# Kernel tuning notes

Measured on AMD Instinct MI355X. Metric: run time of the kernel, lower is better.

The kernel has to match this reference:

```python
import jax, jax.numpy as jnp
import numpy as np

WINDOW_SIZE = 3
SIGMA = 1.5
C1 = 0.01 ** 2
C2 = 0.03 ** 2


def gaussian_window(channel, window_size=WINDOW_SIZE, sigma=SIGMA):
    x = jnp.arange(window_size, dtype=jnp.float32) - window_size // 2
    g1 = jnp.exp(-(x ** 2) / (2.0 * sigma ** 2))
    g1 = g1 / g1.sum()
    g2 = jnp.outer(g1, g1)  # [k, k]
    # depthwise kernel OIHW: [C, 1, k, k]
    return jnp.broadcast_to(g2, (channel, 1, window_size, window_size))


def depthwise_conv(x, window, channel, window_size=WINDOW_SIZE):
    pad = window_size // 2
    return jax.lax.conv_general_dilated(
        x, window,
        window_strides=(1, 1),
        padding=((pad, pad), (pad, pad)),
        dimension_numbers=('NCHW', 'OIHW', 'NCHW'),
        feature_group_count=channel,
    )


def setup_inputs() -> dict:
    key = jax.random.key(0)
    k1, k2 = jax.random.split(key)
    img1 = jax.random.uniform(k1, (32, 3, 512, 512), dtype=jnp.float32)
    img2 = jax.random.uniform(k2, (32, 3, 512, 512), dtype=jnp.float32)
    return {"img1": img1, "img2": img2}


def reference(img1, img2):
    channel = img1.shape[1]
    window = gaussian_window(channel)

    mu1 = depthwise_conv(img1, window, channel)
    mu2 = depthwise_conv(img2, window, channel)
    mu1_sq = mu1 * mu1
    mu2_sq = mu2 * mu2
    mu1_mu2 = mu1 * mu2

    sigma1_sq = depthwise_conv(img1 * img1, window, channel) - mu1_sq
    sigma2_sq = depthwise_conv(img2 * img2, window, channel) - mu2_sq
    sigma12 = depthwise_conv(img1 * img2, window, channel) - mu1_mu2

    ssim_map = ((2.0 * mu1_mu2 + C1) * (2.0 * sigma12 + C2)) / (
        (mu1_sq + mu2_sq + C1) * (sigma1_sq + sigma2_sq + C2))

    # size_sum defaults to True inside ssim() -> scalar sum
    return 1.0 - ssim_map.sum()
```

## Files before the change

kernel.cpp:

```cpp
#include <hip/hip_runtime.h>

#define IMG_H 512
#define IMG_W 512
#define RH 32

__global__ void ssim_init_kernel(double* __restrict__ accum) {
    if (threadIdx.x == 0 && blockIdx.x == 0) *accum = 0.0;
}

__global__ __launch_bounds__(256) void ssim_main_kernel(
    const float* __restrict__ img1, const float* __restrict__ img2,
    double* __restrict__ accum)
{
    constexpr float W_E = 0.30780133f;
    constexpr float W_C = 0.38439734f;
    constexpr float C1 = 1e-4f;
    constexpr float C2 = 9e-4f;

    const int t = threadIdx.x;
    const int y0 = blockIdx.x * RH;
    const size_t base = (size_t)blockIdx.y * (IMG_H * IMG_W);
    const float* __restrict__ A = img1 + base;
    const float* __restrict__ B = img2 + base;

    __shared__ __align__(16) float lsA[2][520];
    __shared__ __align__(16) float lsB[2][520];
    if (t < 2) {
        lsA[0][t * 513] = 0.0f; lsA[1][t * 513] = 0.0f;
        lsB[0][t * 513] = 0.0f; lsB[1][t * 513] = 0.0f;
    }

    const int x = 2 * t;

    float h1[2][3], h2[2][3], h11[2][3], h22[2][3], h12[2][3];
#pragma unroll
    for (int c = 0; c < 2; ++c)
#pragma unroll
        for (int r = 0; r < 3; ++r) {
            h1[c][r] = 0.f; h2[c][r] = 0.f;
            h11[c][r] = 0.f; h22[c][r] = 0.f; h12[c][r] = 0.f;
        }

    float2 pa = make_float2(0.f, 0.f), pb = make_float2(0.f, 0.f);
    {
        const int yi = y0 - 1;
        if (yi >= 0) {
            pa = *(const float2*)(A + (size_t)yi * IMG_W + x);
            pb = *(const float2*)(B + (size_t)yi * IMG_W + x);
        }
    }

    float tsum = 0.0f;

    for (int i = 0; i < RH + 2; ++i) {
        const int buf = i & 1;
        lsA[buf][1 + x] = pa.x; lsA[buf][2 + x] = pa.y;
        lsB[buf][1 + x] = pb.x; lsB[buf][2 + x] = pb.y;

        const int yn = y0 + i;
        float2 na = make_float2(0.f, 0.f), nb = make_float2(0.f, 0.f);
        if (i + 1 < RH + 2 && yn < IMG_H) {
            na = *(const float2*)(A + (size_t)yn * IMG_W + x);
            nb = *(const float2*)(B + (size_t)yn * IMG_W + x);
        }

        __syncthreads();

        const float2 a01 = *(const float2*)&lsA[buf][x];
        const float2 a23 = *(const float2*)&lsA[buf][x + 2];
        const float2 b01 = *(const float2*)&lsB[buf][x];
        const float2 b23 = *(const float2*)&lsB[buf][x + 2];
        const float av[4] = {a01.x, a01.y, a23.x, a23.y};
        const float bv[4] = {b01.x, b01.y, b23.x, b23.y};

#pragma unroll
        for (int c = 0; c < 2; ++c) {
            h1[c][0] = h1[c][1];  h1[c][1] = h1[c][2];
            h2[c][0] = h2[c][1];  h2[c][1] = h2[c][2];
            h11[c][0] = h11[c][1]; h11[c][1] = h11[c][2];
            h22[c][0] = h22[c][1]; h22[c][1] = h22[c][2];
            h12[c][0] = h12[c][1]; h12[c][1] = h12[c][2];
            const float am = av[c], a0 = av[c + 1], ap = av[c + 2];
            const float bm = bv[c], b0 = bv[c + 1], bp = bv[c + 2];
            h1[c][2]  = W_E * (am + ap) + W_C * a0;
            h2[c][2]  = W_E * (bm + bp) + W_C * b0;
            h11[c][2] = W_E * (am * am + ap * ap) + W_C * (a0 * a0);
            h22[c][2] = W_E * (bm * bm + bp * bp) + W_C * (b0 * b0);
            h12[c][2] = W_E * (am * bm + ap * bp) + W_C * (a0 * b0);
        }

        if (i >= 2) {
#pragma unroll
            for (int c = 0; c < 2; ++c) {
                const float mu1 = W_E * (h1[c][0] + h1[c][2]) + W_C * h1[c][1];
                const float mu2 = W_E * (h2[c][0] + h2[c][2]) + W_C * h2[c][1];
                const float e11 = W_E * (h11[c][0] + h11[c][2]) + W_C * h11[c][1];
                const float e22 = W_E * (h22[c][0] + h22[c][2]) + W_C * h22[c][1];
                const float e12 = W_E * (h12[c][0] + h12[c][2]) + W_C * h12[c][1];
                const float mu1s = mu1 * mu1, mu2s = mu2 * mu2, m12 = mu1 * mu2;
                const float s11 = e11 - mu1s, s22 = e22 - mu2s, s12 = e12 - m12;
                const float num = (2.0f * m12 + C1) * (2.0f * s12 + C2);
                const float den = (mu1s + mu2s + C1) * (s11 + s22 + C2);
                tsum += num / den;
            }
        }

        pa = na; pb = nb;
    }

#pragma unroll
    for (int off = 32; off >= 1; off >>= 1)
        tsum += __shfl_xor(tsum, off, 64);

    __shared__ float wpart[4];
    if ((t & 63) == 0) wpart[t >> 6] = tsum;
    __syncthreads();
    if (t == 0) {
        const double bs = (double)wpart[0] + (double)wpart[1] +
                          (double)wpart[2] + (double)wpart[3];
        atomicAdd(accum, bs);
    }
}

__global__ void ssim_fin_kernel(const double* __restrict__ accum,
                                float* __restrict__ out) {
    if (threadIdx.x == 0 && blockIdx.x == 0) out[0] = 1.0f - (float)(*accum);
}

extern "C" void kernel_launch(void* const* d_in, const int* in_sizes, int n_in,
                              void* d_out, int out_size, void* d_ws, size_t ws_size,
                              hipStream_t stream) {
    const float* img1 = (const float*)d_in[0];
    const float* img2 = (const float*)d_in[1];
    float* out = (float*)d_out;
    double* accum = (double*)d_ws;

    const int planes = in_sizes[0] / (IMG_H * IMG_W);

    ssim_init_kernel<<<1, 1, 0, stream>>>(accum);
    dim3 grid(IMG_H / RH, planes);
    ssim_main_kernel<<<grid, 256, 0, stream>>>(img1, img2, accum);
    ssim_fin_kernel<<<1, 1, 0, stream>>>(accum, out);
}
```

Measured before the change: 229.2 us.

## Replace LDS halo exchange with direct global loads and per-block partial sums

Removes the shared-memory row staging and the per-row __syncthreads, so each thread loads its own left and right halo pixels straight from global memory (cache-served). The row loop is unrolled by six with register rotation, which removes the h-array shifts. The double atomic accumulator and its init kernel are replaced by per-block partial writes and a parallel reduction in the final kernel, saving one launch. The trade-off is extra scalar global loads per row, plus a launch_bounds occupancy hint.

```diff
diff --git a/kernel.cpp b/kernel.cpp
--- a/kernel.cpp
+++ b/kernel.cpp
@@ -4,127 +4,138 @@
 #define IMG_W 512
 #define RH 32
 
-__global__ void ssim_init_kernel(double* __restrict__ accum) {
-    if (threadIdx.x == 0 && blockIdx.x == 0) *accum = 0.0;
-}
 
-__global__ __launch_bounds__(256) void ssim_main_kernel(
+__global__ __launch_bounds__(256, 6) void ssim_main_kernel(
     const float* __restrict__ img1, const float* __restrict__ img2,
-    double* __restrict__ accum)
+    double* __restrict__ partial)
 {
     constexpr float W_E = 0.30780133f;
     constexpr float W_C = 0.38439734f;
-    constexpr float C1 = 1e-4f;
-    constexpr float C2 = 9e-4f;
+    constexpr float C1c = 1e-4f;
+    constexpr float C2c = 9e-4f;
 
     const int t = threadIdx.x;
     const int y0 = blockIdx.x * RH;
-    const size_t base = (size_t)blockIdx.y * (IMG_H * IMG_W);
+    const size_t base = (size_t)blockIdx.y * (size_t)(IMG_H * IMG_W);
     const float* __restrict__ A = img1 + base;
     const float* __restrict__ B = img2 + base;
-
-    __shared__ __align__(16) float lsA[2][520];
-    __shared__ __align__(16) float lsB[2][520];
-    if (t < 2) {
-        lsA[0][t * 513] = 0.0f; lsA[1][t * 513] = 0.0f;
-        lsB[0][t * 513] = 0.0f; lsB[1][t * 513] = 0.0f;
-    }
-
+    const bool has_l = (t > 0);
+    const bool has_r = (t < 255);
     const int x = 2 * t;
 
     float h1[2][3], h2[2][3], h11[2][3], h22[2][3], h12[2][3];
-#pragma unroll
-    for (int c = 0; c < 2; ++c)
-#pragma unroll
-        for (int r = 0; r < 3; ++r) {
-            h1[c][r] = 0.f; h2[c][r] = 0.f;
-            h11[c][r] = 0.f; h22[c][r] = 0.f; h12[c][r] = 0.f;
-        }
-
-    float2 pa = make_float2(0.f, 0.f), pb = make_float2(0.f, 0.f);
-    {
-        const int yi = y0 - 1;
-        if (yi >= 0) {
-            pa = *(const float2*)(A + (size_t)yi * IMG_W + x);
-            pb = *(const float2*)(B + (size_t)yi * IMG_W + x);
-        }
-    }
 
     float tsum = 0.0f;
 
-    for (int i = 0; i < RH + 2; ++i) {
-        const int buf = i & 1;
-        lsA[buf][1 + x] = pa.x; lsA[buf][2 + x] = pa.y;
-        lsB[buf][1 + x] = pb.x; lsB[buf][2 + x] = pb.y;
+    float a00, a01, a02, a03, b00, b01, b02, b03;
+    float a10, a11, a12, a13, b10, b11, b12, b13;
 
-        const int yn = y0 + i;
-        float2 na = make_float2(0.f, 0.f), nb = make_float2(0.f, 0.f);
-        if (i + 1 < RH + 2 && yn < IMG_H) {
-            na = *(const float2*)(A + (size_t)yn * IMG_W + x);
-            nb = *(const float2*)(B + (size_t)yn * IMG_W + x);
-        }
+#define LOADROW(AP, BP, OFF) do {                                   \
+    const float2 _ma = *(const float2*)(A + (OFF));                 \
+    const float2 _mb = *(const float2*)(B + (OFF));                 \
+    AP##1 = _ma.x; AP##2 = _ma.y; BP##1 = _mb.x; BP##2 = _mb.y;     \
+    AP##0 = has_l ? A[(OFF) - 1] : 0.0f;                            \
+    AP##3 = has_r ? A[(OFF) + 2] : 0.0f;                            \
+    BP##0 = has_l ? B[(OFF) - 1] : 0.0f;                            \
+    BP##3 = has_r ? B[(OFF) + 2] : 0.0f;                            \
+} while (0)
 
-        __syncthreads();
+#define ZEROROW(AP, BP) do {                                        \
+    AP##0 = 0.f; AP##1 = 0.f; AP##2 = 0.f; AP##3 = 0.f;             \
+    BP##0 = 0.f; BP##1 = 0.f; BP##2 = 0.f; BP##3 = 0.f;             \
+} while (0)
 
-        const float2 a01 = *(const float2*)&lsA[buf][x];
-        const float2 a23 = *(const float2*)&lsA[buf][x + 2];
-        const float2 b01 = *(const float2*)&lsB[buf][x];
-        const float2 b23 = *(const float2*)&lsB[buf][x + 2];
-        const float av[4] = {a01.x, a01.y, a23.x, a23.y};
-        const float bv[4] = {b01.x, b01.y, b23.x, b23.y};
+#define HPASS(AP, BP, S) do {                                               \
+    const float sa0 = AP##0 * AP##0, sa1 = AP##1 * AP##1;                   \
+    const float sa2 = AP##2 * AP##2, sa3 = AP##3 * AP##3;                   \
+    const float sb0 = BP##0 * BP##0, sb1 = BP##1 * BP##1;                   \
+    const float sb2 = BP##2 * BP##2, sb3 = BP##3 * BP##3;                   \
+    const float p0 = AP##0 * BP##0, p1 = AP##1 * BP##1;                     \
+    const float p2 = AP##2 * BP##2, p3 = AP##3 * BP##3;                     \
+    h1[0][S]  = W_E * (AP##0 + AP##2) + W_C * AP##1;                        \
+    h1[1][S]  = W_E * (AP##1 + AP##3) + W_C * AP##2;                        \
+    h2[0][S]  = W_E * (BP##0 + BP##2) + W_C * BP##1;                        \
+    h2[1][S]  = W_E * (BP##1 + BP##3) + W_C * BP##2;                        \
+    h11[0][S] = W_E * (sa0 + sa2) + W_C * sa1;                              \
+    h11[1][S] = W_E * (sa1 + sa3) + W_C * sa2;                              \
+    h22[0][S] = W_E * (sb0 + sb2) + W_C * sb1;                              \
+    h22[1][S] = W_E * (sb1 + sb3) + W_C * sb2;                              \
+    h12[0][S] = W_E * (p0 + p2) + W_C * p1;                                 \
+    h12[1][S] = W_E * (p1 + p3) + W_C * p2;                                 \
+} while (0)
+
+#define VOUT(E0, E1, MID) do {                                              \
+    _Pragma("unroll")                                                       \
+    for (int c = 0; c < 2; ++c) {                                           \
+        const float mu1 = W_E * (h1[c][E0] + h1[c][E1]) + W_C * h1[c][MID]; \
+        const float mu2 = W_E * (h2[c][E0] + h2[c][E1]) + W_C * h2[c][MID]; \
+        const float e11 = W_E * (h11[c][E0] + h11[c][E1]) + W_C * h11[c][MID]; \
+        const float e22 = W_E * (h22[c][E0] + h22[c][E1]) + W_C * h22[c][MID]; \
+        const float e12 = W_E * (h12[c][E0] + h12[c][E1]) + W_C * h12[c][MID]; \
+        const float mu1s = mu1 * mu1, mu2s = mu2 * mu2, m12 = mu1 * mu2;    \
+        const float s11 = e11 - mu1s, s22 = e22 - mu2s, s12 = e12 - m12;    \
+        const float num = (2.0f * m12 + C1c) * (2.0f * s12 + C2c);          \
+        const float den = (mu1s + mu2s + C1c) * (s11 + s22 + C2c);          \
+        tsum += num / den;                                                  \
+    }                                                                       \
+} while (0)
+
+    size_t off = (size_t)y0 * IMG_W + x;
+
+    if (blockIdx.x != 0) LOADROW(a0, b0, off - IMG_W); else ZEROROW(a0, b0);
+    LOADROW(a1, b1, off);
+    HPASS(a0, b0, 0);
+    LOADROW(a0, b0, off + IMG_W);
+    HPASS(a1, b1, 1);
+    off += 2 * (size_t)IMG_W;
+
+#pragma unroll 1
+    for (int g = 0; g < 5; ++g) {
+        LOADROW(a1, b1, off); off += IMG_W; HPASS(a0, b0, 2); VOUT(2, 0, 1);
+        LOADROW(a0, b0, off); off += IMG_W; HPASS(a1, b1, 0); VOUT(0, 1, 2);
+        LOADROW(a1, b1, off); off += IMG_W; HPASS(a0, b0, 1); VOUT(1, 2, 0);
+        LOADROW(a0, b0, off); off += IMG_W; HPASS(a1, b1, 2); VOUT(2, 0, 1);
+        LOADROW(a1, b1, off); off += IMG_W; HPASS(a0, b0, 0); VOUT(0, 1, 2);
+        LOADROW(a0, b0, off); off += IMG_W; HPASS(a1, b1, 1); VOUT(1, 2, 0);
+    }
+
+    if (blockIdx.x != (IMG_H / RH - 1)) LOADROW(a1, b1, off); else ZEROROW(a1, b1);
+    HPASS(a0, b0, 2); VOUT(2, 0, 1);
+    HPASS(a1, b1, 0); VOUT(0, 1, 2);
+
+#undef LOADROW
+#undef ZEROROW
+#undef HPASS
+#undef VOUT
 
 #pragma unroll
-        for (int c = 0; c < 2; ++c) {
-            h1[c][0] = h1[c][1];  h1[c][1] = h1[c][2];
-            h2[c][0] = h2[c][1];  h2[c][1] = h2[c][2];
-            h11[c][0] = h11[c][1]; h11[c][1] = h11[c][2];
-            h22[c][0] = h22[c][1]; h22[c][1] = h22[c][2];
-            h12[c][0] = h12[c][1]; h12[c][1] = h12[c][2];
-            const float am = av[c], a0 = av[c + 1], ap = av[c + 2];
-            const float bm = bv[c], b0 = bv[c + 1], bp = bv[c + 2];
-            h1[c][2]  = W_E * (am + ap) + W_C * a0;
-            h2[c][2]  = W_E * (bm + bp) + W_C * b0;
-            h11[c][2] = W_E * (am * am + ap * ap) + W_C * (a0 * a0);
-            h22[c][2] = W_E * (bm * bm + bp * bp) + W_C * (b0 * b0);
-            h12[c][2] = W_E * (am * bm + ap * bp) + W_C * (a0 * b0);
-        }
-
-        if (i >= 2) {
-#pragma unroll
-            for (int c = 0; c < 2; ++c) {
-                const float mu1 = W_E * (h1[c][0] + h1[c][2]) + W_C * h1[c][1];
-                const float mu2 = W_E * (h2[c][0] + h2[c][2]) + W_C * h2[c][1];
-                const float e11 = W_E * (h11[c][0] + h11[c][2]) + W_C * h11[c][1];
-                const float e22 = W_E * (h22[c][0] + h22[c][2]) + W_C * h22[c][1];
-                const float e12 = W_E * (h12[c][0] + h12[c][2]) + W_C * h12[c][1];
-                const float mu1s = mu1 * mu1, mu2s = mu2 * mu2, m12 = mu1 * mu2;
-                const float s11 = e11 - mu1s, s22 = e22 - mu2s, s12 = e12 - m12;
-                const float num = (2.0f * m12 + C1) * (2.0f * s12 + C2);
-                const float den = (mu1s + mu2s + C1) * (s11 + s22 + C2);
-                tsum += num / den;
-            }
-        }
-
-        pa = na; pb = nb;
-    }
-
-#pragma unroll
-    for (int off = 32; off >= 1; off >>= 1)
-        tsum += __shfl_xor(tsum, off, 64);
+    for (int o = 32; o >= 1; o >>= 1)
+        tsum += __shfl_xor(tsum, o, 64);
 
     __shared__ float wpart[4];
     if ((t & 63) == 0) wpart[t >> 6] = tsum;
     __syncthreads();
     if (t == 0) {
-        const double bs = (double)wpart[0] + (double)wpart[1] +
-                          (double)wpart[2] + (double)wpart[3];
-        atomicAdd(accum, bs);
+        partial[(size_t)blockIdx.y * gridDim.x + blockIdx.x] =
+            (double)wpart[0] + (double)wpart[1] +
+            (double)wpart[2] + (double)wpart[3];
     }
 }
 
-__global__ void ssim_fin_kernel(const double* __restrict__ accum,
-                                float* __restrict__ out) {
-    if (threadIdx.x == 0 && blockIdx.x == 0) out[0] = 1.0f - (float)(*accum);
+__global__ __launch_bounds__(256) void ssim_fin_kernel(
+    const double* __restrict__ partial, float* __restrict__ out, int n)
+{
+    const int t = threadIdx.x;
+    double s = 0.0;
+    for (int i = t; i < n; i += 256) s += partial[i];
+#pragma unroll
+    for (int o = 32; o >= 1; o >>= 1)
+        s += __shfl_xor(s, o, 64);
+    __shared__ double w[4];
+    if ((t & 63) == 0) w[t >> 6] = s;
+    __syncthreads();
+    if (t == 0)
+        out[0] = 1.0f - (float)(w[0] + w[1] + w[2] + w[3]);
 }
 
 extern "C" void kernel_launch(void* const* d_in, const int* in_sizes, int n_in,
@@ -133,12 +144,12 @@
     const float* img1 = (const float*)d_in[0];
     const float* img2 = (const float*)d_in[1];
     float* out = (float*)d_out;
-    double* accum = (double*)d_ws;
+    double* partial = (double*)d_ws;
 
     const int planes = in_sizes[0] / (IMG_H * IMG_W);
+    const int nblk = IMG_H / RH;
 
-    ssim_init_kernel<<<1, 1, 0, stream>>>(accum);
-    dim3 grid(IMG_H / RH, planes);
-    ssim_main_kernel<<<grid, 256, 0, stream>>>(img1, img2, accum);
-    ssim_fin_kernel<<<1, 1, 0, stream>>>(accum, out);
+    dim3 grid(nblk, planes);
+    ssim_main_kernel<<<grid, 256, 0, stream>>>(img1, img2, partial);
+    ssim_fin_kernel<<<1, 256, 0, stream>>>(partial, out, nblk * planes);
 }
```

Measured after the change: 249.0 us. 8.6% more time.
